# Kernel optimization log

Hardware: AMD Instinct MI355X
Metric: run time of the kernel (lower is better)

The kernel has to match this reference:

```python
import jax, jax.numpy as jnp
import numpy as np

T = 120  # hard-coded timestep count in the original forward


def gru_scan(x, W_ih, W_hh, b_ih, b_hh):
    """Run a torch-style GRUCell over time. x: [B, T, D] -> outputs [B, T, H]."""
    B = x.shape[0]
    H = W_hh.shape[1]

    def step(h, xt):
        gi = xt @ W_ih.T + b_ih          # [B, 3H]
        gh = h @ W_hh.T + b_hh           # [B, 3H]
        i_r, i_z, i_n = jnp.split(gi, 3, axis=-1)
        h_r, h_z, h_n = jnp.split(gh, 3, axis=-1)
        r = jax.nn.sigmoid(i_r + h_r)
        z = jax.nn.sigmoid(i_z + h_z)
        n = jnp.tanh(i_n + r * h_n)
        h_new = (1.0 - z) * n + z * h
        return h_new, h_new

    h0 = jnp.zeros((B, H), x.dtype)
    _, ys = jax.lax.scan(step, h0, jnp.swapaxes(x, 0, 1))  # ys: [T, B, H]
    return jnp.swapaxes(ys, 0, 1)


def setup_inputs() -> dict:
    key = jax.random.key(0)
    ks = jax.random.split(key, 20)
    B, Dc, Da, H, A = 2048, 128, 96, 256, 40
    s = 0.05
    inp = {
        "crime_input": jax.random.normal(ks[0], (B, T, Dc), jnp.float32),
        "anomaly_input": jax.random.normal(ks[1], (B, T, Da), jnp.float32),
        # gru_crime
        "W_ih_c": jax.random.normal(ks[2], (3 * H, Dc), jnp.float32) * s,
        "W_hh_c": jax.random.normal(ks[3], (3 * H, H), jnp.float32) * s,
        "b_ih_c": jax.random.normal(ks[4], (3 * H,), jnp.float32) * s,
        "b_hh_c": jax.random.normal(ks[5], (3 * H,), jnp.float32) * s,
        # gru_anomaly
        "W_ih_a": jax.random.normal(ks[6], (3 * H, Da), jnp.float32) * s,
        "W_hh_a": jax.random.normal(ks[7], (3 * H, H), jnp.float32) * s,
        "b_ih_a": jax.random.normal(ks[8], (3 * H,), jnp.float32) * s,
        "b_hh_a": jax.random.normal(ks[9], (3 * H,), jnp.float32) * s,
        # gru_inter (input = 2H)
        "W_ih_i": jax.random.normal(ks[10], (3 * H, 2 * H), jnp.float32) * s,
        "W_hh_i": jax.random.normal(ks[11], (3 * H, H), jnp.float32) * s,
        "b_ih_i": jax.random.normal(ks[12], (3 * H,), jnp.float32) * s,
        "b_hh_i": jax.random.normal(ks[13], (3 * H,), jnp.float32) * s,
        # attention
        "Wv": jax.random.normal(ks[14], (A, H), jnp.float32) * s,
        "bv": jax.random.normal(ks[15], (A,), jnp.float32) * s,
        "wu": jax.random.normal(ks[16], (A,), jnp.float32) * s,
    }
    return inp


def reference(crime_input, anomaly_input,
              W_ih_c, W_hh_c, b_ih_c, b_hh_c,
              W_ih_a, W_hh_a, b_ih_a, b_hh_a,
              W_ih_i, W_hh_i, b_ih_i, b_hh_i,
              Wv, bv, wu):
    # dropout layers are identity in eval mode
    out_c = gru_scan(crime_input, W_ih_c, W_hh_c, b_ih_c, b_hh_c)      # [B,T,H]
    out_a = gru_scan(anomaly_input, W_ih_a, W_hh_a, b_ih_a, b_hh_a)    # [B,T,H]
    inp_i = jnp.concatenate([out_c, out_a], axis=2)                    # [B,T,2H]
    out_i = gru_scan(inp_i, W_ih_i, W_hh_i, b_ih_i, b_hh_i)            # [B,T,H]

    um = jnp.tanh(jnp.einsum('bth,ah->bta', out_i, Wv) + bv)           # [B,T,A]
    scores = jnp.einsum('bta,a->bt', um, wu)                           # [B,T]
    alpha = jax.nn.softmax(scores, axis=1)                             # [B,T]
    context = jnp.einsum('bt,bth->bh', alpha, out_i)[:, None, :]       # [B,1,H]
    return context
```

## Files before the change

### kernel.cpp

```cpp
#include <hip/hip_runtime.h>

typedef float  f32x4  __attribute__((ext_vector_type(4)));
typedef short  short8 __attribute__((ext_vector_type(8)));
typedef __bf16 bf16x8 __attribute__((ext_vector_type(8)));

#define B_SZ 2048
#define T_SZ 120
#define H_SZ 256
#define G3   768
#define A_SZ 40

#define MFMA_BF16 __builtin_amdgcn_mfma_f32_16x16x32_bf16

union U8 { short8 s; bf16x8 b; };
__device__ __forceinline__ bf16x8 as_bf(short8 s){ U8 u; u.s = s; return u.b; }

__device__ __forceinline__ unsigned short f2bf(float x){
  unsigned u = __float_as_uint(x);
  return (unsigned short)((u + 0x7FFFu + ((u >> 16) & 1u)) >> 16);
}
__device__ __forceinline__ float bf2f(unsigned short h){
  return __uint_as_float(((unsigned)h) << 16);
}
__device__ __forceinline__ void cvt_hilo(float x, short& hi, short& lo){
  unsigned short h = f2bf(x);
  hi = (short)h;
  lo = (short)f2bf(x - bf2f(h));
}
__device__ __forceinline__ float sigm(float x){ return 1.0f / (1.0f + __expf(-x)); }
__device__ __forceinline__ float tanh_(float x){
  float a = fabsf(x);
  float t = 1.0f - 2.0f / (__expf(2.0f * a) + 1.0f);
  return copysignf(t, x);
}

__global__ void zinit(float* __restrict__ p, size_t n){
  size_t i = (size_t)blockIdx.x * 256 + threadIdx.x;
  size_t stride = (size_t)gridDim.x * 256;
  for (; i < n; i += stride) p[i] = 0.0f;
}

__global__ void packall(const float* __restrict__ WihC, const float* __restrict__ WhhC,
                        const float* __restrict__ WihA, const float* __restrict__ WhhA,
                        const float* __restrict__ WihI, const float* __restrict__ WhhI,
                        const float* __restrict__ Wv,
                        short* __restrict__ pIhC, short* __restrict__ pHhC,
                        short* __restrict__ pIhA, short* __restrict__ pHhA,
                        short* __restrict__ pIhI, short* __restrict__ pHhI,
                        short* __restrict__ pWvT)
{
  int b = blockIdx.x;
  int lane = threadIdx.x;
  const float* src; short* dst; int K;
  if      (b < 192)  { src = WihC; dst = pIhC; K = 128; }
  else if (b < 576)  { b -= 192;  src = WhhC; dst = pHhC; K = 256; }
  else if (b < 720)  { b -= 576;  src = WihA; dst = pIhA; K = 96;  }
  else if (b < 1104) { b -= 720;  src = WhhA; dst = pHhA; K = 256; }
  else if (b < 1872) { b -= 1104; src = WihI; dst = pIhI; K = 512; }
  else if (b < 2256) { b -= 1872; src = WhhI; dst = pHhI; K = 256; }
  else {
    int bb = b - 2256;
    int q = bb >> 3, kt = bb & 7;
    int a = q * 16 + (lane & 15);
    int k = kt * 32 + (lane >> 4) * 8;
    size_t o = (((size_t)q * 8 + kt) * 64 + lane) * 8;
#pragma unroll
    for (int i = 0; i < 8; i++){
      float v = (a < A_SZ) ? Wv[(size_t)a * H_SZ + k + i] : 0.0f;
      pWvT[o + i] = (short)f2bf(v);
    }
    return;
  }
  int KT = K >> 5;
  int nt = b / KT, kt = b % KT;
  const float* s = src + (size_t)(nt * 16 + (lane & 15)) * K + kt * 32 + (lane >> 4) * 8;
  size_t o = (((size_t)nt * KT + kt) * 64 + lane) * 8;
#pragma unroll
  for (int i = 0; i < 8; i++) dst[o + i] = (short)f2bf(s[i]);
}

__device__ __forceinline__ void gemm_body(
    int bid, const short* __restrict__ A, const short* __restrict__ Bhi,
    const float* __restrict__ b1, const float* __restrict__ b2,
    float* __restrict__ C, short* Ash)
{
  int tid = threadIdx.x;
  int w = tid >> 6, lane = tid & 63;
  int mg = w & 1, ng = w >> 1;
  int m0 = bid * 64;
  int nb = ng * 12;
  const int KT = 16;

  {
    int r = tid >> 3, s0 = (tid & 7) * 64;
    const short* src = A + (size_t)(m0 + r) * 512 + s0;
    short* dst = Ash + r * 520 + s0;
#pragma unroll
    for (int i = 0; i < 8; i++)
      *(short8*)(dst + i * 8) = *(const short8*)(src + i * 8);
  }
  __syncthreads();

  const f32x4 zero = {0.f, 0.f, 0.f, 0.f};
  f32x4 acc[2][12];
#pragma unroll
  for (int f = 0; f < 2; f++)
#pragma unroll
    for (int q = 0; q < 12; q++) acc[f][q] = zero;

  int rr = lane & 15, ks = lane >> 4;
  const short* Ap[2];
#pragma unroll
  for (int f = 0; f < 2; f++)
    Ap[f] = Ash + (mg * 32 + f * 16 + rr) * 520 + ks * 8;

  for (int kt = 0; kt < KT; ++kt){
    bf16x8 ahb[2];
#pragma unroll
    for (int f = 0; f < 2; f++)
      ahb[f] = as_bf(*(const short8*)(Ap[f] + kt * 32));
#pragma unroll
    for (int q = 0; q < 12; q++){
      int bo = (((nb + q) * KT + kt) * 64 + lane) * 8;
      bf16x8 bh = as_bf(*(const short8*)(Bhi + bo));
#pragma unroll
      for (int f = 0; f < 2; f++)
        acc[f][q] = MFMA_BF16(ahb[f], bh, acc[f][q], 0, 0, 0);
    }
  }
  int nc = lane & 15;
  int rb = lane >> 4;
#pragma unroll
  for (int q = 0; q < 12; q++){
    int n = (nb + q) * 16 + nc;
    float bias = b1[n] + (n < 512 ? b2[n] : 0.0f);
#pragma unroll
    for (int f = 0; f < 2; f++)
#pragma unroll
      for (int i = 0; i < 4; i++)
        C[(size_t)(m0 + mg * 32 + f * 16 + rb * 4 + i) * G3 + n] = acc[f][q][i] + bias;
  }
}

template<int D, int KI>
__device__ __forceinline__ void leaf32_body(
    const float* __restrict__ x, const short* __restrict__ Wih,
    const short* __restrict__ Whh, const float* __restrict__ bih,
    const float* __restrict__ bhh, short* __restrict__ outp, int ooff,
    float* __restrict__ hs, int b0, int t0, int tcnt,
    short* hhi, short* hlo, short* xhi)
{
  constexpr int XP  = D + 8;
  constexpr int NST = 4 * D;
  constexpr int CPR = D / 8;
  int tid = threadIdx.x, w = tid >> 6, lane = tid & 63;
  int arow = lane & 15, kgrp = lane >> 4;
  int c0 = w * 16 + arow;
  int msk = (arow & 7) << 4;

  float bir[2], biz[2], bin_[2], bhn[2];
#pragma unroll
  for (int j = 0; j < 2; j++){
    int c = c0 + j * 128;
    bir[j] = bih[c] + bhh[c];
    biz[j] = bih[256 + c] + bhh[256 + c];
    bin_[j] = bih[512 + c];
    bhn[j] = bhh[512 + c];
  }

  int srow = tid / CPR, scol = (tid % CPR) * 8;
  bool stg = tid < NST;
  const float* sx = x + ((size_t)(b0 + srow) * T_SZ + t0) * D + scol;
  short* xwh = xhi + srow * XP + scol;

  int orow = tid >> 4, ocb = (tid & 15) * 16;
  const char* ord0 = (const char*)hhi + orow * 512 + ((ocb * 2) ^ ((orow & 7) << 4));
  const char* ord1 = (const char*)hhi + orow * 512 + (((ocb + 8) * 2) ^ ((orow & 7) << 4));
  short* owp = outp + (size_t)(b0 + orow) * tcnt * 512 + ooff + ocb;

  float hreg[2][2][4];
#pragma unroll
  for (int f = 0; f < 2; f++)
#pragma unroll
  for (int j = 0; j < 2; j++)
#pragma unroll
  for (int i = 0; i < 4; i++){
    int row = f * 16 + kgrp * 4 + i, c = c0 + j * 128;
    float v = hs[(size_t)(b0 + row) * H_SZ + c];
    hreg[f][j][i] = v;
    short h_, l_; cvt_hilo(v, h_, l_);
    int off = row * 512 + ((c * 2) ^ ((row & 7) << 4));
    *(short*)((char*)hhi + off) = h_;
    *(short*)((char*)hlo + off) = l_;
  }
  if (stg){
    f32x4 a0 = *(const f32x4*)sx;
    f32x4 a1 = *(const f32x4*)(sx + 4);
    short8 h8;
#pragma unroll
    for (int i = 0; i < 4; i++){ h8[i] = (short)f2bf(a0[i]); h8[4+i] = (short)f2bf(a1[i]); }
    *(short8*)xwh = h8;
  }
  __syncthreads();

  const char *hhp[2], *hlp[2], *xhp[2];
#pragma unroll
  for (int f = 0; f < 2; f++){
    hhp[f] = (const char*)hhi + (f * 16 + arow) * 512;
    hlp[f] = (const char*)hlo + (f * 16 + arow) * 512;
    xhp[f] = (const char*)xhi + ((f * 16 + arow) * XP + kgrp * 8) * 2;
  }

  const f32x4 zero = {0.f, 0.f, 0.f, 0.f};
  for (int t = 0; t < tcnt; t++){
    if (t > 0){
      *(short8*)(owp + (size_t)(t - 1) * 512) = *(const short8*)ord0;
      *(short8*)(owp + (size_t)(t - 1) * 512 + 8) = *(const short8*)ord1;
    }

    f32x4 acc[2][6], accNi[2][2];
#pragma unroll
    for (int f = 0; f < 2; f++){
#pragma unroll
      for (int q = 0; q < 6; q++) acc[f][q] = zero;
      accNi[f][0] = zero; accNi[f][1] = zero;
    }

#pragma unroll
    for (int kt = 0; kt < KI; kt++){
      short8 wb[6];
#pragma unroll
      for (int q = 0; q < 6; q++)
        wb[q] = *(const short8*)(Wih + (((w + 8 * q) * KI + kt) * 64 + lane) * 8);
      bf16x8 ah[2];
#pragma unroll
      for (int f = 0; f < 2; f++)
        ah[f] = as_bf(*(const short8*)(xhp[f] + kt * 64));
#pragma unroll
      for (int q = 0; q < 6; q++){
        bf16x8 bw = as_bf(wb[q]);
#pragma unroll
        for (int f = 0; f < 2; f++){
          if (q < 4) acc[f][q] = MFMA_BF16(ah[f], bw, acc[f][q], 0, 0, 0);
          else       accNi[f][q-4] = MFMA_BF16(ah[f], bw, accNi[f][q-4], 0, 0, 0);
        }
      }
    }
#pragma unroll
    for (int kt = 0; kt < 8; kt++){
      short8 wb[6];
#pragma unroll
      for (int q = 0; q < 6; q++)
        wb[q] = *(const short8*)(Whh + (((w + 8 * q) * 8 + kt) * 64 + lane) * 8);
      int kb = (kt * 64 + kgrp * 16) ^ msk;
      bf16x8 ah[2], al[2];
#pragma unroll
      for (int f = 0; f < 2; f++){
        ah[f] = as_bf(*(const short8*)(hhp[f] + kb));
        al[f] = as_bf(*(const short8*)(hlp[f] + kb));
      }
#pragma unroll
      for (int q = 0; q < 6; q++){
        bf16x8 bw = as_bf(wb[q]);
#pragma unroll
        for (int f = 0; f < 2; f++){
          acc[f][q] = MFMA_BF16(ah[f], bw, acc[f][q], 0, 0, 0);
          acc[f][q] = MFMA_BF16(al[f], bw, acc[f][q], 0, 0, 0);
        }
      }
    }
    __syncthreads();

    f32x4 a0, a1;
    bool ds = stg && (t + 1 < tcnt);
    if (ds){
      a0 = *(const f32x4*)(sx + (size_t)(t + 1) * D);
      a1 = *(const f32x4*)(sx + (size_t)(t + 1) * D + 4);
    }

#pragma unroll
    for (int f = 0; f < 2; f++)
#pragma unroll
    for (int j = 0; j < 2; j++)
#pragma unroll
    for (int i = 0; i < 4; i++){
      float rr = sigm(acc[f][j][i] + bir[j]);
      float zz = sigm(acc[f][2 + j][i] + biz[j]);
      float nn = tanh_(accNi[f][j][i] + bin_[j] + rr * (acc[f][4 + j][i] + bhn[j]));
      float hv = (1.0f - zz) * nn + zz * hreg[f][j][i];
      hreg[f][j][i] = hv;
      int row = f * 16 + kgrp * 4 + i, c = c0 + j * 128;
      short h_, l_; cvt_hilo(hv, h_, l_);
      int off = row * 512 + ((c * 2) ^ ((row & 7) << 4));
      *(short*)((char*)hhi + off) = h_;
      *(short*)((char*)hlo + off) = l_;
    }
    if (ds){
      short8 h8;
#pragma unroll
      for (int i = 0; i < 4; i++){ h8[i] = (short)f2bf(a0[i]); h8[4+i] = (short)f2bf(a1[i]); }
      *(short8*)xwh = h8;
    }
    __syncthreads();
  }

  *(short8*)(owp + (size_t)(tcnt - 1) * 512) = *(const short8*)ord0;
  *(short8*)(owp + (size_t)(tcnt - 1) * 512 + 8) = *(const short8*)ord1;

#pragma unroll
  for (int f = 0; f < 2; f++)
#pragma unroll
  for (int j = 0; j < 2; j++)
#pragma unroll
  for (int i = 0; i < 4; i++){
    int row = f * 16 + kgrp * 4 + i;
    hs[(size_t)(b0 + row) * H_SZ + c0 + j * 128] = hreg[f][j][i];
  }
}

__device__ __forceinline__ void inter_body(
    int bid, const float* __restrict__ gi,
    const short* __restrict__ Whh, const float* __restrict__ bhh,
    const short* __restrict__ WvT,
    const float* __restrict__ bv, const float* __restrict__ wu,
    float* __restrict__ ctx, float* __restrict__ lsum,
    float* __restrict__ hs, int tcnt,
    short* hhi, short* hlo, short* wvl, float* esh)
{
  int b0 = bid * 16;
  int tid = threadIdx.x, w = tid >> 6, lane = tid & 63;
  int arow = lane & 15, kgrp = lane >> 4;
  int c0 = w * 16 + arow;
  int msk = (arow & 7) << 4;

  float bhn[2];
  bhn[0] = bhh[512 + c0];
  bhn[1] = bhh[512 + c0 + 128];

  float wuv[3], bvv[3];
#pragma unroll
  for (int q = 0; q < 3; q++){
    int a = q * 16 + arow;
    wuv[q] = (a < A_SZ) ? wu[a] : 0.0f;
    bvv[q] = (a < A_SZ) ? bv[a] : 0.0f;
  }

  for (int i = tid; i < 3 * 8 * 64; i += 512)
    *(short8*)(wvl + i * 8) = *(const short8*)(WvT + (size_t)i * 8);

  float hreg[2][4];
#pragma unroll
  for (int j = 0; j < 2; j++)
#pragma unroll
  for (int i = 0; i < 4; i++){
    int row = kgrp * 4 + i, c = c0 + j * 128;
    float v = hs[(size_t)(b0 + row) * H_SZ + c];
    hreg[j][i] = v;
    short h_, l_; cvt_hilo(v, h_, l_);
    int off = row * 512 + ((c * 2) ^ ((row & 7) << 4));
    *(short*)((char*)hhi + off) = h_;
    *(short*)((char*)hlo + off) = l_;
  }
  __syncthreads();

  const char* hhp = (const char*)hhi + arow * 512;
  const char* hlp = (const char*)hlo + arow * 512;
  const float* gp[4];
#pragma unroll
  for (int i = 0; i < 4; i++)
    gp[i] = gi + (size_t)(b0 + kgrp * 4 + i) * tcnt * G3;

  float ctxa[2][4] = {{0.f,0.f,0.f,0.f},{0.f,0.f,0.f,0.f}};
  float lsr[4] = {0.f, 0.f, 0.f, 0.f};

  const f32x4 zero = {0.f, 0.f, 0.f, 0.f};
  for (int t = 0; t < tcnt; t++){
    float gvr[2][4], gvz[2][4], gvn[2][4];
#pragma unroll
    for (int j = 0; j < 2; j++)
#pragma unroll
    for (int i = 0; i < 4; i++){
      const float* g = gp[i] + (size_t)t * G3 + c0 + j * 128;
      gvr[j][i] = g[0];
      gvz[j][i] = g[256];
      gvn[j][i] = g[512];
    }

    f32x4 acc[6];
#pragma unroll
    for (int q = 0; q < 6; q++) acc[q] = zero;

    short8 wb[6], wn[6];
#pragma unroll
    for (int q = 0; q < 6; q++)
      wb[q] = *(const short8*)(Whh + (((w + 8 * q) * 8) * 64 + lane) * 8);
#pragma unroll
    for (int kt = 0; kt < 8; kt++){
      if (kt < 7){
#pragma unroll
        for (int q = 0; q < 6; q++)
          wn[q] = *(const short8*)(Whh + (((w + 8 * q) * 8 + kt + 1) * 64 + lane) * 8);
      }
      int kb = (kt * 64 + kgrp * 16) ^ msk;
      bf16x8 ah = as_bf(*(const short8*)(hhp + kb));
      bf16x8 al = as_bf(*(const short8*)(hlp + kb));
#pragma unroll
      for (int q = 0; q < 6; q++){
        bf16x8 bw = as_bf(wb[q]);
        acc[q] = MFMA_BF16(ah, bw, acc[q], 0, 0, 0);
        acc[q] = MFMA_BF16(al, bw, acc[q], 0, 0, 0);
      }
      if (kt < 7){
#pragma unroll
        for (int q = 0; q < 6; q++) wb[q] = wn[q];
      }
    }

    if (w == 0 && t > 0){
      f32x4 um[3];
#pragma unroll
      for (int q = 0; q < 3; q++) um[q] = zero;
#pragma unroll
      for (int kt = 0; kt < 8; kt++){
        int kb = (kt * 64 + kgrp * 16) ^ msk;
        bf16x8 ah = as_bf(*(const short8*)(hhp + kb));
#pragma unroll
        for (int q = 0; q < 3; q++){
          bf16x8 bw = as_bf(*(const short8*)(wvl + ((q * 8 + kt) * 64 + lane) * 8));
          um[q] = MFMA_BF16(ah, bw, um[q], 0, 0, 0);
        }
      }
      f32x4 sp;
#pragma unroll
      for (int i = 0; i < 4; i++){
        float v = 0.f;
#pragma unroll
        for (int q = 0; q < 3; q++)
          v += wuv[q] * tanh_(um[q][i] + bvv[q]);
        sp[i] = v;
      }
#pragma unroll
      for (int d = 1; d < 16; d <<= 1){
#pragma unroll
        for (int i = 0; i < 4; i++)
          sp[i] += __shfl_xor(sp[i], d);
      }
      if (arow == 0){
#pragma unroll
        for (int i = 0; i < 4; i++){
          float e = __expf(sp[i]);
          esh[kgrp * 4 + i] = e;
          lsr[i] += e;
        }
      }
    }
    __syncthreads();

    if (t > 0){
#pragma unroll
      for (int i = 0; i < 4; i++){
        float e = esh[kgrp * 4 + i];
#pragma unroll
        for (int j = 0; j < 2; j++)
          ctxa[j][i] += e * hreg[j][i];
      }
    }

#pragma unroll
    for (int j = 0; j < 2; j++)
#pragma unroll
    for (int i = 0; i < 4; i++){
      float rr = sigm(gvr[j][i] + acc[j][i]);
      float zz = sigm(gvz[j][i] + acc[2 + j][i]);
      float nn = tanh_(gvn[j][i] + rr * (acc[4 + j][i] + bhn[j]));
      float hv = (1.0f - zz) * nn + zz * hreg[j][i];
      hreg[j][i] = hv;
      int row = kgrp * 4 + i, c = c0 + j * 128;
      short h_, l_; cvt_hilo(hv, h_, l_);
      int off = row * 512 + ((c * 2) ^ ((row & 7) << 4));
      *(short*)((char*)hhi + off) = h_;
      *(short*)((char*)hlo + off) = l_;
    }
    __syncthreads();
  }

  if (w == 0){
    f32x4 um[3];
#pragma unroll
    for (int q = 0; q < 3; q++) um[q] = zero;
#pragma unroll
    for (int kt = 0; kt < 8; kt++){
      int kb = (kt * 64 + kgrp * 16) ^ msk;
      bf16x8 ah = as_bf(*(const short8*)(hhp + kb));
#pragma unroll
      for (int q = 0; q < 3; q++){
        bf16x8 bw = as_bf(*(const short8*)(wvl + ((q * 8 + kt) * 64 + lane) * 8));
        um[q] = MFMA_BF16(ah, bw, um[q], 0, 0, 0);
      }
    }
    f32x4 sp;
#pragma unroll
    for (int i = 0; i < 4; i++){
      float v = 0.f;
#pragma unroll
      for (int q = 0; q < 3; q++)
        v += wuv[q] * tanh_(um[q][i] + bvv[q]);
      sp[i] = v;
    }
#pragma unroll
    for (int d = 1; d < 16; d <<= 1){
#pragma unroll
      for (int i = 0; i < 4; i++)
        sp[i] += __shfl_xor(sp[i], d);
    }
    if (arow == 0){
#pragma unroll
      for (int i = 0; i < 4; i++){
        float e = __expf(sp[i]);
        esh[kgrp * 4 + i] = e;
        lsr[i] += e;
      }
    }
  }
  __syncthreads();
#pragma unroll
  for (int i = 0; i < 4; i++){
    float e = esh[kgrp * 4 + i];
#pragma unroll
    for (int j = 0; j < 2; j++)
      ctxa[j][i] += e * hreg[j][i];
  }

#pragma unroll
  for (int j = 0; j < 2; j++)
#pragma unroll
  for (int i = 0; i < 4; i++){
    int row = kgrp * 4 + i;
    hs[(size_t)(b0 + row) * H_SZ + c0 + j * 128] = hreg[j][i];
    ctx[(size_t)(b0 + row) * H_SZ + c0 + j * 128] += ctxa[j][i];
  }
  if (w == 0 && arow == 0){
#pragma unroll
    for (int i = 0; i < 4; i++)
      lsum[b0 + kgrp * 4 + i] += lsr[i];
  }
}

__global__ __launch_bounds__(512, 2) void fused3(
    int nIb, int nLb,
    const float* __restrict__ giI, const short* __restrict__ WhhI_,
    const float* __restrict__ bhhI_, const short* __restrict__ WvT,
    const float* __restrict__ bv, const float* __restrict__ wu,
    float* __restrict__ ctx, float* __restrict__ lsum,
    float* __restrict__ hsI, int tcntI,
    const float* __restrict__ x0, const short* __restrict__ WihL0,
    const short* __restrict__ WhhL0, const float* __restrict__ bihL0,
    const float* __restrict__ bhhL0,
    const float* __restrict__ x1, const short* __restrict__ WihL1,
    const short* __restrict__ WhhL1, const float* __restrict__ bihL1,
    const float* __restrict__ bhhL1,
    short* __restrict__ outL, float* __restrict__ hsC, float* __restrict__ hsA,
    int t0L, int tcntL,
    const short* __restrict__ Ag, const short* __restrict__ BhiG,
    const float* __restrict__ b1G, const float* __restrict__ b2G,
    float* __restrict__ Cg)
{
  __shared__ short smem[64 * 520];
  int bid = blockIdx.x;
  if (bid < nIb){
    inter_body(bid, giI, WhhI_, bhhI_, WvT, bv, wu, ctx, lsum, hsI, tcntI,
               smem, smem + 4096, smem + 8192, (float*)(smem + 20480));
  } else if (bid < nIb + nLb){
    int lb = bid - nIb;
    short* hhi = smem;
    short* hlo = smem + 8192;
    short* xhi = smem + 16384;
    if (lb < 64)
      leaf32_body<128, 4>(x0, WihL0, WhhL0, bihL0, bhhL0, outL, 0, hsC,
                          lb * 32, t0L, tcntL, hhi, hlo, xhi);
    else
      leaf32_body<96, 3>(x1, WihL1, WhhL1, bihL1, bhhL1, outL, 256, hsA,
                         (lb - 64) * 32, t0L, tcntL, hhi, hlo, xhi);
  } else {
    gemm_body(bid - nIb - nLb, Ag, BhiG, b1G, b2G, Cg, smem);
  }
}

__global__ __launch_bounds__(256, 1) void attn_fin(
    const float* __restrict__ ctx, const float* __restrict__ lsum,
    float* __restrict__ out)
{
  int b = blockIdx.x, tid = threadIdx.x;
  out[(size_t)b * H_SZ + tid] = ctx[(size_t)b * H_SZ + tid] / lsum[b];
}

extern "C" void kernel_launch(void* const* d_in, const int* in_sizes, int n_in,
                              void* d_out, int out_size, void* d_ws, size_t ws_size,
                              hipStream_t stream)
{
  (void)in_sizes; (void)n_in; (void)out_size;
  const float* crime = (const float*)d_in[0];
  const float* anom  = (const float*)d_in[1];
  const float* WihC = (const float*)d_in[2];
  const float* WhhC = (const float*)d_in[3];
  const float* bihC = (const float*)d_in[4];
  const float* bhhC = (const float*)d_in[5];
  const float* WihA = (const float*)d_in[6];
  const float* WhhA = (const float*)d_in[7];
  const float* bihA = (const float*)d_in[8];
  const float* bhhA = (const float*)d_in[9];
  const float* WihI = (const float*)d_in[10];
  const float* WhhI = (const float*)d_in[11];
  const float* bihI = (const float*)d_in[12];
  const float* bhhI = (const float*)d_in[13];
  const float* Wv = (const float*)d_in[14];
  const float* bv = (const float*)d_in[15];
  const float* wu = (const float*)d_in[16];
  float* out = (float*)d_out;

  char* ws = (char*)d_ws;
  size_t off = 0;
  auto take = [&](size_t n){ size_t r = off; off += (n + 255) & ~(size_t)255; return r; };

  short* pIhC = (short*)(ws + take((size_t)G3 * 128 * 2));
  short* pHhC = (short*)(ws + take((size_t)G3 * 256 * 2));
  short* pIhA = (short*)(ws + take((size_t)G3 * 96 * 2));
  short* pHhA = (short*)(ws + take((size_t)G3 * 256 * 2));
  short* pIhI = (short*)(ws + take((size_t)G3 * 512 * 2));
  short* pHhI = (short*)(ws + take((size_t)G3 * 256 * 2));
  short* pWvT = (short*)(ws + take((size_t)3 * 8 * 64 * 8 * 2));

  size_t state_off = off;
  float* hsC  = (float*)(ws + take((size_t)B_SZ * H_SZ * 4));
  float* hsA  = (float*)(ws + take((size_t)B_SZ * H_SZ * 4));
  float* hsI  = (float*)(ws + take((size_t)B_SZ * H_SZ * 4));
  float* ctx  = (float*)(ws + take((size_t)B_SZ * H_SZ * 4));
  float* lsum = (float*)(ws + take((size_t)B_SZ * 4));
  size_t state_end = off;

  size_t per2 = (size_t)B_SZ * (G3 * 4 + 512 * 2) * 2;
  size_t avail = (ws_size > off + 8192) ? (ws_size - off - 8192) : 0;
  int TC = (int)(avail / per2);
  if (TC > 12) TC = 12;
  if (TC < 1) TC = 1;
  if (TC > T_SZ) TC = T_SZ;
  int nc = (T_SZ + TC - 1) / TC;

  float* Gi[2];  short* OcaH[2];
  Gi[0]   = (float*)(ws + take((size_t)B_SZ * TC * G3 * 4));
  Gi[1]   = (float*)(ws + take((size_t)B_SZ * TC * G3 * 4));
  OcaH[0] = (short*)(ws + take((size_t)B_SZ * TC * 512 * 2));
  OcaH[1] = (short*)(ws + take((size_t)B_SZ * TC * 512 * 2));

  auto tcn = [&](int j){
    if (j < 0 || j >= nc) return 0;
    int r = T_SZ - j * TC;
    return r < TC ? r : TC;
  };

  zinit<<<2048, 256, 0, stream>>>((float*)(ws + state_off), (state_end - state_off) / 4);
  packall<<<2280, 64, 0, stream>>>(WihC, WhhC, WihA, WhhA, WihI, WhhI, Wv,
                                   pIhC, pHhC, pIhA, pHhA, pIhI, pHhI, pWvT);

  for (int k = 0; k <= nc + 1; k++){
    int tL = tcn(k), tG = tcn(k - 1), tI = tcn(k - 2);
    int nLb = tL ? 128 : 0;
    int nGb = tG ? (B_SZ * tG) / 64 : 0;
    int nIb = tI ? 128 : 0;
    int grid = nIb + nLb + nGb;
    if (grid == 0) continue;
    fused3<<<grid, 512, 0, stream>>>(
        nIb, nLb,
        Gi[k & 1], pHhI, bhhI, pWvT, bv, wu, ctx, lsum, hsI, tI,
        crime, pIhC, pHhC, bihC, bhhC,
        anom,  pIhA, pHhA, bihA, bhhA,
        OcaH[k & 1], hsC, hsA, k * TC, tL,
        OcaH[(k - 1) & 1], pIhI, bihI, bhhI, Gi[(k - 1) & 1]);
  }
  attn_fin<<<B_SZ, 256, 0, stream>>>(ctx, lsum, out);
}
```

Measured before the change: 3.160 ms.

## Fuse inter-GRU input projection into recurrent loop, drop separate GEMM stage

Removes the separate gemm stage that precomputed the inter-layer input gates into a float Gi buffer. The inter block now computes x·W_ih inside the time loop with bf16 MFMA on activations staged through shared memory, prefetching the next timestep's input while the gates are computed. This cuts the pipeline from three stages to two and drops the large fp32 Gi traffic. In exchange it adds per-timestep work on the serial recurrent critical path of the 128 inter blocks.

```diff
diff --git a/kernel.cpp b/kernel.cpp
--- a/kernel.cpp
+++ b/kernel.cpp
@@ -79,69 +79,6 @@
   for (int i = 0; i < 8; i++) dst[o + i] = (short)f2bf(s[i]);
 }
 
-__device__ __forceinline__ void gemm_body(
-    int bid, const short* __restrict__ A, const short* __restrict__ Bhi,
-    const float* __restrict__ b1, const float* __restrict__ b2,
-    float* __restrict__ C, short* Ash)
-{
-  int tid = threadIdx.x;
-  int w = tid >> 6, lane = tid & 63;
-  int mg = w & 1, ng = w >> 1;
-  int m0 = bid * 64;
-  int nb = ng * 12;
-  const int KT = 16;
-
-  {
-    int r = tid >> 3, s0 = (tid & 7) * 64;
-    const short* src = A + (size_t)(m0 + r) * 512 + s0;
-    short* dst = Ash + r * 520 + s0;
-#pragma unroll
-    for (int i = 0; i < 8; i++)
-      *(short8*)(dst + i * 8) = *(const short8*)(src + i * 8);
-  }
-  __syncthreads();
-
-  const f32x4 zero = {0.f, 0.f, 0.f, 0.f};
-  f32x4 acc[2][12];
-#pragma unroll
-  for (int f = 0; f < 2; f++)
-#pragma unroll
-    for (int q = 0; q < 12; q++) acc[f][q] = zero;
-
-  int rr = lane & 15, ks = lane >> 4;
-  const short* Ap[2];
-#pragma unroll
-  for (int f = 0; f < 2; f++)
-    Ap[f] = Ash + (mg * 32 + f * 16 + rr) * 520 + ks * 8;
-
-  for (int kt = 0; kt < KT; ++kt){
-    bf16x8 ahb[2];
-#pragma unroll
-    for (int f = 0; f < 2; f++)
-      ahb[f] = as_bf(*(const short8*)(Ap[f] + kt * 32));
-#pragma unroll
-    for (int q = 0; q < 12; q++){
-      int bo = (((nb + q) * KT + kt) * 64 + lane) * 8;
-      bf16x8 bh = as_bf(*(const short8*)(Bhi + bo));
-#pragma unroll
-      for (int f = 0; f < 2; f++)
-        acc[f][q] = MFMA_BF16(ahb[f], bh, acc[f][q], 0, 0, 0);
-    }
-  }
-  int nc = lane & 15;
-  int rb = lane >> 4;
-#pragma unroll
-  for (int q = 0; q < 12; q++){
-    int n = (nb + q) * 16 + nc;
-    float bias = b1[n] + (n < 512 ? b2[n] : 0.0f);
-#pragma unroll
-    for (int f = 0; f < 2; f++)
-#pragma unroll
-      for (int i = 0; i < 4; i++)
-        C[(size_t)(m0 + mg * 32 + f * 16 + rb * 4 + i) * G3 + n] = acc[f][q][i] + bias;
-  }
-}
-
 template<int D, int KI>
 __device__ __forceinline__ void leaf32_body(
     const float* __restrict__ x, const short* __restrict__ Wih,
@@ -318,14 +255,15 @@
   }
 }
 
-__device__ __forceinline__ void inter_body(
-    int bid, const float* __restrict__ gi,
-    const short* __restrict__ Whh, const float* __restrict__ bhh,
+__device__ __forceinline__ void interf_body(
+    int bid, const short* __restrict__ xh,
+    const short* __restrict__ Wih, const short* __restrict__ Whh,
+    const float* __restrict__ bih, const float* __restrict__ bhh,
     const short* __restrict__ WvT,
     const float* __restrict__ bv, const float* __restrict__ wu,
     float* __restrict__ ctx, float* __restrict__ lsum,
     float* __restrict__ hs, int tcnt,
-    short* hhi, short* hlo, short* wvl, float* esh)
+    short* hhi, short* hlo, short* xq, short* wvl, float* esh)
 {
   int b0 = bid * 16;
   int tid = threadIdx.x, w = tid >> 6, lane = tid & 63;
@@ -333,9 +271,15 @@
   int c0 = w * 16 + arow;
   int msk = (arow & 7) << 4;
 
-  float bhn[2];
-  bhn[0] = bhh[512 + c0];
-  bhn[1] = bhh[512 + c0 + 128];
+  float bir[2], biz[2], bin_[2], bhn[2];
+#pragma unroll
+  for (int j = 0; j < 2; j++){
+    int c = c0 + j * 128;
+    bir[j] = bih[c] + bhh[c];
+    biz[j] = bih[256 + c] + bhh[256 + c];
+    bin_[j] = bih[512 + c];
+    bhn[j] = bhh[512 + c];
+  }
 
   float wuv[3], bvv[3];
 #pragma unroll
@@ -347,6 +291,10 @@
 
   for (int i = tid; i < 3 * 8 * 64; i += 512)
     *(short8*)(wvl + i * 8) = *(const short8*)(WvT + (size_t)i * 8);
+
+  int srow = tid >> 5, scol = (tid & 31) * 16;
+  const short* sx = xh + (size_t)(b0 + srow) * tcnt * 512 + scol;
+  short* xw = xq + srow * 520 + scol;
 
   float hreg[2][4];
 #pragma unroll
@@ -361,46 +309,44 @@
     *(short*)((char*)hhi + off) = h_;
     *(short*)((char*)hlo + off) = l_;
   }
+  *(short8*)xw = *(const short8*)sx;
+  *(short8*)(xw + 8) = *(const short8*)(sx + 8);
   __syncthreads();
 
   const char* hhp = (const char*)hhi + arow * 512;
   const char* hlp = (const char*)hlo + arow * 512;
-  const float* gp[4];
-#pragma unroll
-  for (int i = 0; i < 4; i++)
-    gp[i] = gi + (size_t)(b0 + kgrp * 4 + i) * tcnt * G3;
+  const short* xqp = xq + arow * 520 + kgrp * 8;
 
   float ctxa[2][4] = {{0.f,0.f,0.f,0.f},{0.f,0.f,0.f,0.f}};
   float lsr[4] = {0.f, 0.f, 0.f, 0.f};
 
   const f32x4 zero = {0.f, 0.f, 0.f, 0.f};
   for (int t = 0; t < tcnt; t++){
-    float gvr[2][4], gvz[2][4], gvn[2][4];
-#pragma unroll
-    for (int j = 0; j < 2; j++)
-#pragma unroll
-    for (int i = 0; i < 4; i++){
-      const float* g = gp[i] + (size_t)t * G3 + c0 + j * 128;
-      gvr[j][i] = g[0];
-      gvz[j][i] = g[256];
-      gvn[j][i] = g[512];
-    }
-
-    f32x4 acc[6];
+    f32x4 acc[6], accNi[2];
 #pragma unroll
     for (int q = 0; q < 6; q++) acc[q] = zero;
-
-    short8 wb[6], wn[6];
-#pragma unroll
-    for (int q = 0; q < 6; q++)
-      wb[q] = *(const short8*)(Whh + (((w + 8 * q) * 8) * 64 + lane) * 8);
+    accNi[0] = zero; accNi[1] = zero;
+
+#pragma unroll
+    for (int kt = 0; kt < 16; kt++){
+      short8 wb[6];
+#pragma unroll
+      for (int q = 0; q < 6; q++)
+        wb[q] = *(const short8*)(Wih + (((w + 8 * q) * 16 + kt) * 64 + lane) * 8);
+      bf16x8 ah = as_bf(*(const short8*)(xqp + kt * 32));
+#pragma unroll
+      for (int q = 0; q < 6; q++){
+        bf16x8 bw = as_bf(wb[q]);
+        if (q < 4) acc[q] = MFMA_BF16(ah, bw, acc[q], 0, 0, 0);
+        else       accNi[q-4] = MFMA_BF16(ah, bw, accNi[q-4], 0, 0, 0);
+      }
+    }
 #pragma unroll
     for (int kt = 0; kt < 8; kt++){
-      if (kt < 7){
-#pragma unroll
-        for (int q = 0; q < 6; q++)
-          wn[q] = *(const short8*)(Whh + (((w + 8 * q) * 8 + kt + 1) * 64 + lane) * 8);
-      }
+      short8 wb[6];
+#pragma unroll
+      for (int q = 0; q < 6; q++)
+        wb[q] = *(const short8*)(Whh + (((w + 8 * q) * 8 + kt) * 64 + lane) * 8);
       int kb = (kt * 64 + kgrp * 16) ^ msk;
       bf16x8 ah = as_bf(*(const short8*)(hhp + kb));
       bf16x8 al = as_bf(*(const short8*)(hlp + kb));
@@ -409,10 +355,6 @@
         bf16x8 bw = as_bf(wb[q]);
         acc[q] = MFMA_BF16(ah, bw, acc[q], 0, 0, 0);
         acc[q] = MFMA_BF16(al, bw, acc[q], 0, 0, 0);
-      }
-      if (kt < 7){
-#pragma unroll
-        for (int q = 0; q < 6; q++) wb[q] = wn[q];
       }
     }
 
@@ -466,13 +408,20 @@
       }
     }
 
+    short8 a0s, a1s;
+    bool ds = (t + 1 < tcnt);
+    if (ds){
+      a0s = *(const short8*)(sx + (size_t)(t + 1) * 512);
+      a1s = *(const short8*)(sx + (size_t)(t + 1) * 512 + 8);
+    }
+
 #pragma unroll
     for (int j = 0; j < 2; j++)
 #pragma unroll
     for (int i = 0; i < 4; i++){
-      float rr = sigm(gvr[j][i] + acc[j][i]);
-      float zz = sigm(gvz[j][i] + acc[2 + j][i]);
-      float nn = tanh_(gvn[j][i] + rr * (acc[4 + j][i] + bhn[j]));
+      float rr = sigm(acc[j][i] + bir[j]);
+      float zz = sigm(acc[2 + j][i] + biz[j]);
+      float nn = tanh_(accNi[j][i] + bin_[j] + rr * (acc[4 + j][i] + bhn[j]));
       float hv = (1.0f - zz) * nn + zz * hreg[j][i];
       hreg[j][i] = hv;
       int row = kgrp * 4 + i, c = c0 + j * 128;
@@ -481,6 +430,10 @@
       *(short*)((char*)hhi + off) = h_;
       *(short*)((char*)hlo + off) = l_;
     }
+    if (ds){
+      *(short8*)xw = a0s;
+      *(short8*)(xw + 8) = a1s;
+    }
     __syncthreads();
   }
 
@@ -546,9 +499,10 @@
   }
 }
 
-__global__ __launch_bounds__(512, 2) void fused3(
-    int nIb, int nLb,
-    const float* __restrict__ giI, const short* __restrict__ WhhI_,
+__global__ __launch_bounds__(512, 2) void fused2(
+    int nIb,
+    const short* __restrict__ xhI, const short* __restrict__ WihI_,
+    const short* __restrict__ WhhI_, const float* __restrict__ bihI_,
     const float* __restrict__ bhhI_, const short* __restrict__ WvT,
     const float* __restrict__ bv, const float* __restrict__ wu,
     float* __restrict__ ctx, float* __restrict__ lsum,
@@ -560,17 +514,16 @@
     const short* __restrict__ WhhL1, const float* __restrict__ bihL1,
     const float* __restrict__ bhhL1,
     short* __restrict__ outL, float* __restrict__ hsC, float* __restrict__ hsA,
-    int t0L, int tcntL,
-    const short* __restrict__ Ag, const short* __restrict__ BhiG,
-    const float* __restrict__ b1G, const float* __restrict__ b2G,
-    float* __restrict__ Cg)
+    int t0L, int tcntL)
 {
-  __shared__ short smem[64 * 520];
+  __shared__ short smem[28864];
   int bid = blockIdx.x;
   if (bid < nIb){
-    inter_body(bid, giI, WhhI_, bhhI_, WvT, bv, wu, ctx, lsum, hsI, tcntI,
-               smem, smem + 4096, smem + 8192, (float*)(smem + 20480));
-  } else if (bid < nIb + nLb){
+    interf_body(bid, xhI, WihI_, WhhI_, bihI_, bhhI_, WvT, bv, wu,
+                ctx, lsum, hsI, tcntI,
+                smem, smem + 4096, smem + 8192, smem + 16512,
+                (float*)(smem + 28800));
+  } else {
     int lb = bid - nIb;
     short* hhi = smem;
     short* hlo = smem + 8192;
@@ -581,8 +534,6 @@
     else
       leaf32_body<96, 3>(x1, WihL1, WhhL1, bihL1, bhhL1, outL, 256, hsA,
                          (lb - 64) * 32, t0L, tcntL, hhi, hlo, xhi);
-  } else {
-    gemm_body(bid - nIb - nLb, Ag, BhiG, b1G, b2G, Cg, smem);
   }
 }
 
@@ -638,7 +589,7 @@
   float* lsum = (float*)(ws + take((size_t)B_SZ * 4));
   size_t state_end = off;
 
-  size_t per2 = (size_t)B_SZ * (G3 * 4 + 512 * 2) * 2;
+  size_t per2 = (size_t)B_SZ * (512 * 2) * 2;
   size_t avail = (ws_size > off + 8192) ? (ws_size - off - 8192) : 0;
   int TC = (int)(avail / per2);
   if (TC > 12) TC = 12;
@@ -646,9 +597,7 @@
   if (TC > T_SZ) TC = T_SZ;
   int nc = (T_SZ + TC - 1) / TC;
 
-  float* Gi[2];  short* OcaH[2];
-  Gi[0]   = (float*)(ws + take((size_t)B_SZ * TC * G3 * 4));
-  Gi[1]   = (float*)(ws + take((size_t)B_SZ * TC * G3 * 4));
+  short* OcaH[2];
   OcaH[0] = (short*)(ws + take((size_t)B_SZ * TC * 512 * 2));
   OcaH[1] = (short*)(ws + take((size_t)B_SZ * TC * 512 * 2));
 
@@ -662,20 +611,19 @@
   packall<<<2280, 64, 0, stream>>>(WihC, WhhC, WihA, WhhA, WihI, WhhI, Wv,
                                    pIhC, pHhC, pIhA, pHhA, pIhI, pHhI, pWvT);
 
-  for (int k = 0; k <= nc + 1; k++){
-    int tL = tcn(k), tG = tcn(k - 1), tI = tcn(k - 2);
+  for (int k = 0; k <= nc; k++){
+    int tL = tcn(k), tI = tcn(k - 1);
     int nLb = tL ? 128 : 0;
-    int nGb = tG ? (B_SZ * tG) / 64 : 0;
     int nIb = tI ? 128 : 0;
-    int grid = nIb + nLb + nGb;
+    int grid = nIb + nLb;
     if (grid == 0) continue;
-    fused3<<<grid, 512, 0, stream>>>(
-        nIb, nLb,
-        Gi[k & 1], pHhI, bhhI, pWvT, bv, wu, ctx, lsum, hsI, tI,
+    fused2<<<grid, 512, 0, stream>>>(
+        nIb,
+        OcaH[(k - 1) & 1], pIhI, pHhI, bihI, bhhI, pWvT, bv, wu,
+        ctx, lsum, hsI, tI,
         crime, pIhC, pHhC, bihC, bhhC,
         anom,  pIhA, pHhA, bihA, bhhA,
-        OcaH[k & 1], hsC, hsA, k * TC, tL,
-        OcaH[(k - 1) & 1], pIhI, bihI, bhhI, Gi[(k - 1) & 1]);
+        OcaH[k & 1], hsC, hsA, k * TC, tL);
   }
   attn_fin<<<B_SZ, 256, 0, stream>>>(ctx, lsum, out);
 }
```

Measured after the change: 6.485 ms. 2.05x slower.
